# Kernel tuning notes

Measured on AMD Instinct MI355X. Metric: run time of the kernel, lower is better.

The kernel has to match this reference:

```python
import jax, jax.numpy as jnp
import numpy as np

B, T_LAT = 64, 1024
K, PAD = 15, 7
# SMPL-style parents for 24 joints (joint 0 = root)
PARENTS = [0, 0, 0, 0, 1, 2, 3, 4, 5, 6, 7, 8, 9, 9, 9, 12, 13, 14, 16, 17, 18, 19, 20, 21]


def _fine_adjacency():
    # edges of the kinematic tree; +1 virtual root-displacement node (Aberman find_neighbor, dist=1)
    edges = [(PARENTS[j], j) for j in range(1, 24)]  # 23 edges
    n = len(edges) + 1  # 24 graph nodes
    A = np.eye(n, dtype=bool)
    for i, (pi, ci) in enumerate(edges):
        for j, (pj, cj) in enumerate(edges):
            if {pi, ci} & {pj, cj}:
                A[i, j] = True
        if pi == 0 or ci == 0:  # edges touching the root neighbor the virtual root node
            A[i, n - 1] = A[n - 1, i] = True
    return A


def _coarsen(A, pools):
    m = len(pools)
    Ac = np.eye(m, dtype=bool)
    for a in range(m):
        for b in range(m):
            if A[np.ix_(pools[a], pools[b])].any():
                Ac[a, b] = True
    return Ac


def _unpool_weight(pools, n_fine, cpj):
    # SkeletonUnpool: binary matrix copying each coarse joint's channels to its fine members
    W = np.zeros((n_fine * cpj, len(pools) * cpj), np.float32)
    for i, grp in enumerate(pools):
        for j in grp:
            for c in range(cpj):
                W[j * cpj + c, i * cpj + c] = 1.0
    return W


def _conv_mask(A, in_cpj, out_cpj, k):
    n = A.shape[0]
    M = np.zeros((n * out_cpj, n * in_cpj, k), np.float32)
    for a in range(n):
        for b in range(n):
            if A[a, b]:
                M[a * out_cpj:(a + 1) * out_cpj, b * in_cpj:(b + 1) * in_cpj, :] = 1.0
    return M


def _lin_mask(A, in_cpj, out_cpj):
    n = A.shape[0]
    M = np.zeros((n * out_cpj, n * in_cpj), np.float32)
    for a in range(n):
        for b in range(n):
            if A[a, b]:
                M[a * out_cpj:(a + 1) * out_cpj, b * in_cpj:(b + 1) * in_cpj] = 1.0
    return M


def setup_inputs() -> dict:
    key = jax.random.key(0)
    ks = jax.random.split(key, 12)
    A0 = _fine_adjacency()                           # 24 fine graph nodes
    P0 = [[2 * i, 2 * i + 1] for i in range(12)]     # pooling 24 -> 12
    P1 = [[2 * i, 2 * i + 1] for i in range(6)]      # pooling 12 -> 6
    A1 = _coarsen(A0, P0)                            # 12-node coarse adjacency

    inp = {
        'x': jax.random.normal(ks[0], (B, T_LAT, 96), jnp.float32),      # latent: 6 joints x 16 ch
        'offset0': jax.random.normal(ks[1], (B, 12, 3), jnp.float32),
        'offset1': jax.random.normal(ks[2], (B, 24, 3), jnp.float32),
        'W_unpool0': jnp.asarray(_unpool_weight(P1, 12, 16)),            # (192, 96)
        'W_unpool1': jnp.asarray(_unpool_weight(P0, 24, 8)),             # (192, 96)
        'conv_w0': jax.random.normal(ks[3], (96, 192, K), jnp.float32) * 0.05,
        'conv_b0': jax.random.normal(ks[4], (96,), jnp.float32) * 0.05,
        'conv_w1': jax.random.normal(ks[5], (96, 192, K), jnp.float32) * 0.05,
        'conv_b1': jax.random.normal(ks[6], (96,), jnp.float32) * 0.05,
        'off_w0': jax.random.normal(ks[7], (96, 36), jnp.float32) * 0.05,
        'off_b0': jax.random.normal(ks[8], (96,), jnp.float32) * 0.05,
        'off_w1': jax.random.normal(ks[9], (96, 72), jnp.float32) * 0.05,
        'off_b1': jax.random.normal(ks[10], (96,), jnp.float32) * 0.05,
        'conv_mask0': jnp.asarray(_conv_mask(A1, 16, 8, K)),
        'conv_mask1': jnp.asarray(_conv_mask(A0, 8, 4, K)),
        'off_mask0': jnp.asarray(_lin_mask(A1, 3, 8)),
        'off_mask1': jnp.asarray(_lin_mask(A0, 3, 4)),
    }
    return inp


def _upsample2(h):
    # nn.Upsample(scale_factor=2, mode='linear', align_corners=False) on last axis
    b, c, t = h.shape
    return jax.image.resize(h, (b, c, 2 * t), method='linear')


def _conv1d(h, w, b):
    y = jax.lax.conv_general_dilated(h, w, (1,), [(PAD, PAD)],
                                     dimension_numbers=('NCH', 'OIH', 'NCH'))
    return y + b[None, :, None]


def reference(x, offset0, offset1, W_unpool0, W_unpool1,
              conv_w0, conv_b0, conv_w1, conv_b1,
              off_w0, off_b0, off_w1, off_b1,
              conv_mask0, conv_mask1, off_mask0, off_mask1):
    h = jnp.swapaxes(x, -2, -1)                       # (B, C_lat, T)
    # ---- stage 0: upsample time, unpool 6->12 joints, masked conv, offset, LeakyReLU
    h = _upsample2(h)
    h = jnp.einsum('oc,bct->bot', W_unpool0, h)       # (B, 192, 2T)
    h = _conv1d(h, conv_w0 * conv_mask0, conv_b0)     # (B, 96, 2T)
    off = offset0.reshape(offset0.shape[0], -1) @ (off_w0 * off_mask0).T + off_b0
    h = h + off[:, :, None] / 100.0
    h = jax.nn.leaky_relu(h, 0.2)
    # ---- stage 1 (last layer: no activation)
    h = _upsample2(h)
    h = jnp.einsum('oc,bct->bot', W_unpool1, h)       # (B, 192, 4T)
    h = _conv1d(h, conv_w1 * conv_mask1, conv_b1)     # (B, 96, 4T)
    off = offset1.reshape(offset1.shape[0], -1) @ (off_w1 * off_mask1).T + off_b1
    h = h + off[:, :, None] / 100.0
    return h[:, :, :-1]                               # trim last frame
```

## Files before the change

### kernel.cpp

```cpp
#include <hip/hip_runtime.h>

typedef unsigned short ushort_t;
typedef unsigned int u32;
typedef short bf16x8 __attribute__((ext_vector_type(8)));
typedef float f32x4 __attribute__((ext_vector_type(4)));
typedef u32 u32x4 __attribute__((ext_vector_type(4)));

__device__ __forceinline__ float bf2f(ushort_t u) {
    u32 x = ((u32)u) << 16; float f; __builtin_memcpy(&f, &x, 4); return f;
}
__device__ __forceinline__ ushort_t f2bf(float f) {
    u32 x; __builtin_memcpy(&x, &f, 4);
    x = x + 0x7fffu + ((x >> 16) & 1u);
    return (ushort_t)(x >> 16);
}

#define NBB 128
#define UROWS 136
#define USTRB 208
#define UB_BYTES (UROWS * USTRB)
#define LDS_TOTAL UB_BYTES
#define LSTR1 261

__global__ void prepA(const float* __restrict__ w0, const float* __restrict__ m0,
                      const float* __restrict__ w1, const float* __restrict__ m1,
                      const float* __restrict__ offw0, const float* __restrict__ offb0,
                      const float* __restrict__ omask0, const float* __restrict__ convb0,
                      const float* __restrict__ off0,
                      const float* __restrict__ offw1, const float* __restrict__ offb1,
                      const float* __restrict__ omask1, const float* __restrict__ convb1,
                      const float* __restrict__ off1,
                      float* __restrict__ Wplain, float* __restrict__ ADD0,
                      float* __restrict__ ADD1)
{
    int idx = blockIdx.x * 256 + threadIdx.x;
    if (idx < 18432) {
        int o = idx % 96;
        int cc = (idx / 96) % 96;
        int st = idx / 9216;
        const float* w = st ? w1 : w0;
        const float* mk = st ? m1 : m0;
        int cpj = st ? 8 : 16;
        int i = cc / cpj, c = cc % cpj;
        float s[15];
#pragma unroll
        for (int k = 0; k < 15; ++k) s[k] = 0.f;
#pragma unroll
        for (int d = 0; d < 2; ++d) {
            int f = (2 * i + d) * cpj + c;
            int base = (o * 192 + f) * 15;
#pragma unroll
            for (int k = 0; k < 15; ++k)
                s[k] += w[base + k] * mk[base + k];
        }
#pragma unroll
        for (int k = 0; k < 15; ++k)
            Wplain[st * 138240 + (k * 96 + cc) * 96 + o] = s[k];
    } else if (idx < 18432 + 12288) {
        int a = idx - 18432;
        int st = a / 6144; int a2 = a % 6144;
        int o = a2 % 96, b = a2 / 96;
        const float* ow = st ? offw1 : offw0;
        const float* ob = st ? offb1 : offb0;
        const float* om = st ? omask1 : omask0;
        const float* cb = st ? convb1 : convb0;
        const float* of = st ? off1 : off0;
        int J = st ? 72 : 36;
        float s = 0.f;
        for (int j2 = 0; j2 < J; ++j2) s += ow[o * J + j2] * om[o * J + j2] * of[b * J + j2];
        (st ? ADD1 : ADD0)[b * 96 + o] = cb[o] + (s + ob[o]) * 0.01f;
    }
}

__global__ void prepB(const float* __restrict__ Wplain,
                      ushort_t* __restrict__ Wp0, ushort_t* __restrict__ Wp1)
{
    int idx = blockIdx.x * 256 + threadIdx.x;
    if (idx >= 331776) return;
    int o = idx % 96; int t = idx / 96;
    int cc = t % 96; t /= 96;
    int j = t % 9; t /= 9;
    int p = t % 2; int st = t / 2;
    const float* WP = Wplain + (size_t)st * 138240;
    int kk[4]; float cf[4];
    if (p == 0) { kk[0]=2*j;   cf[0]=0.75f; kk[1]=2*j-2; cf[1]=0.25f;
                  kk[2]=2*j+1; cf[2]=0.25f; kk[3]=2*j-1; cf[3]=0.75f; }
    else        { kk[0]=2*j;   cf[0]=0.25f; kk[1]=2*j-2; cf[1]=0.75f;
                  kk[2]=2*j-1; cf[2]=0.75f; kk[3]=2*j-3; cf[3]=0.25f; }
    float s = 0.f;
#pragma unroll
    for (int q = 0; q < 4; ++q) {
        int k = kk[q];
        if (k >= 0 && k < 15) s += cf[q] * WP[(k * 96 + cc) * 96 + o];
    }
    int lane = (o & 15) | (((cc >> 3) & 3) << 4);
    int mh = (o >> 4) / 3, m = (o >> 4) % 3;
    int pos = ((((j * 2 + mh) * 2 + p) * 9) + (cc >> 5) * 3 + m) * 512 + lane * 8 + (cc & 7);
    (st ? Wp1 : Wp0)[pos] = f2bf(s);
}

template<int BF16SRC>
__global__ void prep_G(const float* __restrict__ WP, const float* __restrict__ srcF,
                       const ushort_t* __restrict__ srcB, float* __restrict__ G, int T)
{
    int idx = blockIdx.x * 256 + threadIdx.x;
    if (idx >= 184320) return;
    int o = idx % 96; int t = idx / 96;
    int k = t % 15; t /= 15;
    int side = t % 2; int b = t / 2;
    const float* wk = WP + (size_t)k * 9216 + o;
    int row = side ? T - 1 : 0;
    float s = 0.f;
    if (BF16SRC) {
        const ushort_t* xr = srcB + ((size_t)b * T + row) * 96;
        for (int cc = 0; cc < 96; ++cc)
            s += wk[cc * 96] * bf2f(xr[cc]);
    } else {
        const float* xr = srcF + ((size_t)b * T + row) * 96;
        for (int cc = 0; cc < 96; ++cc)
            s += wk[cc * 96] * bf2f(f2bf(xr[cc]));
    }
    G[((size_t)(b * 96 + o) * 15 + k) * 2 + side] = s;
}

__global__ void prep_cfb(const float* __restrict__ G, float* __restrict__ CF,
                         float* __restrict__ CB)
{
    int idx = blockIdx.x * 256 + threadIdx.x;
    if (idx >= 86016) return;
    int seg = idx % 14; int r = idx / 14;
    int o = r % 96; int b = r / 96;
    bool front = seg < 7; int t = front ? seg : seg - 7;
    float s = 0.f;
    if (front) { for (int k = 0; k <= 6 - t; ++k)   s += G[(((size_t)(b*96+o)*15)+k)*2 + 0]; }
    else       { for (int k = 14 - t; k <= 14; ++k) s += G[(((size_t)(b*96+o)*15)+k)*2 + 1]; }
    (front ? CF : CB)[(b * 7 + t) * 96 + o] = s;
}

template<int STAGE>
__launch_bounds__(256, 4)
__global__ void conv_poly(const float* __restrict__ Xf, const ushort_t* __restrict__ Hbf,
                          const ushort_t* __restrict__ Wp, const float* __restrict__ ADD,
                          const float* __restrict__ CF, const float* __restrict__ CB,
                          ushort_t* __restrict__ Hout, float* __restrict__ Fout, int T)
{
    extern __shared__ char smem[];
    char* Ub = smem;

    const int tid = threadIdx.x;
    const int lane = tid & 63;
    const int wid = tid >> 6;
    const int b = blockIdx.y;
    const int tg = blockIdx.x;
    const int mh = blockIdx.z;
    const int phase = wid & 1;
    const int nq = wid >> 1;
    const int rb0 = tg * NBB - 4;

    const ushort_t* wgl = Wp + (size_t)(mh * 2 + phase) * 4608 + lane * 8;

    if (STAGE == 0) {
        const float* xb = Xf + (size_t)b * T * 96;
        for (int idx = tid; idx < UROWS * 12; idx += 256) {
            int r = idx / 12, q = idx - r * 12;
            int rg = rb0 + r; rg = rg < 0 ? 0 : (rg > T - 1 ? T - 1 : rg);
            const float* src = xb + (size_t)rg * 96 + q * 8;
            float4 a = *(const float4*)src;
            float4 c2 = *(const float4*)(src + 4);
            u32x4 v;
            v[0] = (u32)f2bf(a.x) | ((u32)f2bf(a.y) << 16);
            v[1] = (u32)f2bf(a.z) | ((u32)f2bf(a.w) << 16);
            v[2] = (u32)f2bf(c2.x) | ((u32)f2bf(c2.y) << 16);
            v[3] = (u32)f2bf(c2.z) | ((u32)f2bf(c2.w) << 16);
            *(u32x4*)(Ub + r * USTRB + q * 16) = v;
        }
    } else {
        const ushort_t* xb = Hbf + (size_t)b * T * 96;
        for (int idx = tid; idx < UROWS * 12; idx += 256) {
            int r = idx / 12, q = idx - r * 12;
            int rg = rb0 + r; rg = rg < 0 ? 0 : (rg > T - 1 ? T - 1 : rg);
            u32x4 v = *(const u32x4*)(xb + (size_t)rg * 96 + q * 8);
            *(u32x4*)(Ub + r * USTRB + q * 16) = v;
        }
    }
    __syncthreads();

    f32x4 acc[3][4];
#pragma unroll
    for (int m = 0; m < 3; ++m)
#pragma unroll
        for (int n = 0; n < 4; ++n) acc[m][n] = (f32x4){0.f, 0.f, 0.f, 0.f};

    const int rowbase = 64 * nq + (lane & 15);
    const int og16 = (lane >> 4) * 16;

#pragma unroll
    for (int j = 0; j < 9; ++j) {
        const ushort_t* wj = wgl + (size_t)j * 18432;
        bf16x8 aj[9];
#pragma unroll
        for (int q = 0; q < 9; ++q)
            aj[q] = *(const bf16x8*)(wj + q * 512);

        const int bj = (rowbase + j) * USTRB;
#pragma unroll
        for (int cb = 0; cb < 3; ++cb) {
            const int off0 = bj + cb * 64 + og16;
            bf16x8 bfr[4];
#pragma unroll
            for (int n = 0; n < 4; ++n)
                bfr[n] = *(const bf16x8*)(Ub + off0 + n * 16 * USTRB);
#pragma unroll
            for (int m = 0; m < 3; ++m)
#pragma unroll
                for (int n = 0; n < 4; ++n)
                    acc[m][n] = __builtin_amdgcn_mfma_f32_16x16x32_bf16(aj[cb * 3 + m], bfr[n], acc[m][n], 0, 0, 0);
        }
    }

    const int T2 = 2 * T;
    const int t0 = tg * 2 * NBB;
    const int og4 = (lane >> 4) * 4;

    __syncthreads();

    if (STAGE == 0) {
        ushort_t* L0 = (ushort_t*)Ub;
#pragma unroll
        for (int m = 0; m < 3; ++m) {
            int obase = mh * 48 + m * 16 + og4;
            float addv[4];
#pragma unroll
            for (int rr = 0; rr < 4; ++rr) addv[rr] = ADD[b * 96 + obase + rr];
#pragma unroll
            for (int n = 0; n < 4; ++n) {
                int tl = 2 * (rowbase + 16 * n) + phase;
                int tgl = t0 + tl;
                ushort_t pk[4];
#pragma unroll
                for (int rr = 0; rr < 4; ++rr) {
                    float v = acc[m][n][rr] + addv[rr];
                    if (tgl < 7)                   v -= CF[(b * 7 + tgl) * 96 + obase + rr];
                    if (tgl >= T2 - 7 && tgl < T2) v -= CB[(b * 7 + tgl - (T2 - 7)) * 96 + obase + rr];
                    v = v > 0.f ? v : 0.2f * v;
                    pk[rr] = f2bf(v);
                }
                uint2 w2;
                w2.x = (u32)pk[0] | ((u32)pk[1] << 16);
                w2.y = (u32)pk[2] | ((u32)pk[3] << 16);
                *(uint2*)((char*)L0 + tl * 104 + (m * 16 + og4) * 2) = w2;
            }
        }
        __syncthreads();
        for (int g = tid; g < 256 * 6; g += 256) {
            int row = g / 6, col = g % 6;
            int t = t0 + row;
            if (t < T2) {
                u32x4 v = *(const u32x4*)((char*)L0 + row * 104 + col * 16);
                *(u32x4*)((char*)Hout + ((size_t)(b * T2 + t) * 96 + mh * 48) * 2 + col * 16) = v;
            }
        }
    } else {
        const int TO = T2 - 1;
        float* L1 = (float*)Ub;
#pragma unroll
        for (int m = 0; m < 3; ++m) {
            int obase = mh * 48 + m * 16 + og4;
            float addv[4];
#pragma unroll
            for (int rr = 0; rr < 4; ++rr) addv[rr] = ADD[b * 96 + obase + rr];
#pragma unroll
            for (int n = 0; n < 4; ++n) {
                int tl = 2 * (rowbase + 16 * n) + phase;
                int tgl = t0 + tl;
#pragma unroll
                for (int rr = 0; rr < 4; ++rr) {
                    float v = acc[m][n][rr] + addv[rr];
                    if (tgl < 7)                   v -= CF[(b * 7 + tgl) * 96 + obase + rr];
                    if (tgl >= T2 - 7 && tgl < T2) v -= CB[(b * 7 + tgl - (T2 - 7)) * 96 + obase + rr];
                    L1[(og4 + rr) * LSTR1 + tl] = v;
                }
            }
            __syncthreads();
            for (int g = tid; g < 4096; g += 256) {
                int row = g >> 8, col = g & 255;
                int t = t0 + col;
                if (t < TO) {
                    int o_g = mh * 48 + m * 16 + row;
                    Fout[((size_t)(b * 96 + o_g)) * TO + t] = L1[row * LSTR1 + col];
                }
            }
            __syncthreads();
        }
    }
}

extern "C" void kernel_launch(void* const* d_in, const int* in_sizes, int n_in,
                              void* d_out, int out_size, void* d_ws, size_t ws_size,
                              hipStream_t stream)
{
    const float* x       = (const float*)d_in[0];
    const float* offset0 = (const float*)d_in[1];
    const float* offset1 = (const float*)d_in[2];
    const float* conv_w0 = (const float*)d_in[5];
    const float* conv_b0 = (const float*)d_in[6];
    const float* conv_w1 = (const float*)d_in[7];
    const float* conv_b1 = (const float*)d_in[8];
    const float* off_w0  = (const float*)d_in[9];
    const float* off_b0  = (const float*)d_in[10];
    const float* off_w1  = (const float*)d_in[11];
    const float* off_b1  = (const float*)d_in[12];
    const float* cmask0  = (const float*)d_in[13];
    const float* cmask1  = (const float*)d_in[14];
    const float* omask0  = (const float*)d_in[15];
    const float* omask1  = (const float*)d_in[16];

    char* ws = (char*)d_ws;
    float*    Wplain = (float*)(ws);
    ushort_t* Wp0    = (ushort_t*)(ws + 1105920);
    ushort_t* Wp1    = (ushort_t*)(ws + 1437696);
    float*    ADD0   = (float*)(ws + 1769472);
    float*    ADD1   = (float*)(ws + 1794048);
    float*    CF0    = (float*)(ws + 1818624);
    float*    CB0    = (float*)(ws + 1990656);
    float*    CF1    = (float*)(ws + 2162688);
    float*    CB1    = (float*)(ws + 2334720);
    float*    G0     = (float*)(ws + 2506752);
    float*    G1     = (float*)(ws + 3244032);
    ushort_t* H1     = (ushort_t*)(ws + 3981312);
    float* out = (float*)d_out;

    prepA<<<120, 256, 0, stream>>>(conv_w0, cmask0, conv_w1, cmask1,
                                   off_w0, off_b0, omask0, conv_b0, offset0,
                                   off_w1, off_b1, omask1, conv_b1, offset1,
                                   Wplain, ADD0, ADD1);
    prepB<<<1296, 256, 0, stream>>>(Wplain, Wp0, Wp1);
    prep_G<0><<<720, 256, 0, stream>>>(Wplain, x, nullptr, G0, 1024);
    prep_cfb<<<336, 256, 0, stream>>>(G0, CF0, CB0);

    conv_poly<0><<<dim3(8, 64, 2), 256, LDS_TOTAL, stream>>>(x, nullptr, Wp0, ADD0, CF0, CB0,
                                                             H1, nullptr, 1024);
    prep_G<1><<<720, 256, 0, stream>>>(Wplain + 138240, nullptr, H1, G1, 2048);
    prep_cfb<<<336, 256, 0, stream>>>(G1, CF1, CB1);
    conv_poly<1><<<dim3(16, 64, 2), 256, LDS_TOTAL, stream>>>(nullptr, H1, Wp1, ADD1, CF1, CB1,
                                                              nullptr, out, 2048);
}
```

Measured before the change: 127.3 us.

## Fuse prep kernels, inline boundary corrections, load stage-1 inputs from global directly

```diff
diff --git a/kernel.cpp b/kernel.cpp
--- a/kernel.cpp
+++ b/kernel.cpp
@@ -19,8 +19,8 @@
 #define UROWS 136
 #define USTRB 208
 #define UB_BYTES (UROWS * USTRB)
-#define LDS_TOTAL UB_BYTES
 #define LSTR1 261
+#define LDS1_BYTES (16 * LSTR1 * 4)
 
 __global__ void prepA(const float* __restrict__ w0, const float* __restrict__ m0,
                       const float* __restrict__ w1, const float* __restrict__ m1,
@@ -72,38 +72,12 @@
     }
 }
 
-__global__ void prepB(const float* __restrict__ Wplain,
-                      ushort_t* __restrict__ Wp0, ushort_t* __restrict__ Wp1)
-{
-    int idx = blockIdx.x * 256 + threadIdx.x;
-    if (idx >= 331776) return;
-    int o = idx % 96; int t = idx / 96;
-    int cc = t % 96; t /= 96;
-    int j = t % 9; t /= 9;
-    int p = t % 2; int st = t / 2;
-    const float* WP = Wplain + (size_t)st * 138240;
-    int kk[4]; float cf[4];
-    if (p == 0) { kk[0]=2*j;   cf[0]=0.75f; kk[1]=2*j-2; cf[1]=0.25f;
-                  kk[2]=2*j+1; cf[2]=0.25f; kk[3]=2*j-1; cf[3]=0.75f; }
-    else        { kk[0]=2*j;   cf[0]=0.25f; kk[1]=2*j-2; cf[1]=0.75f;
-                  kk[2]=2*j-1; cf[2]=0.75f; kk[3]=2*j-3; cf[3]=0.25f; }
-    float s = 0.f;
-#pragma unroll
-    for (int q = 0; q < 4; ++q) {
-        int k = kk[q];
-        if (k >= 0 && k < 15) s += cf[q] * WP[(k * 96 + cc) * 96 + o];
-    }
-    int lane = (o & 15) | (((cc >> 3) & 3) << 4);
-    int mh = (o >> 4) / 3, m = (o >> 4) % 3;
-    int pos = ((((j * 2 + mh) * 2 + p) * 9) + (cc >> 5) * 3 + m) * 512 + lane * 8 + (cc & 7);
-    (st ? Wp1 : Wp0)[pos] = f2bf(s);
-}
-
 template<int BF16SRC>
-__global__ void prep_G(const float* __restrict__ WP, const float* __restrict__ srcF,
-                       const ushort_t* __restrict__ srcB, float* __restrict__ G, int T)
-{
-    int idx = blockIdx.x * 256 + threadIdx.x;
+__device__ __forceinline__ void gbody(int idx, const float* __restrict__ WP,
+                                      const float* __restrict__ srcF,
+                                      const ushort_t* __restrict__ srcB,
+                                      float* __restrict__ G, int T)
+{
     if (idx >= 184320) return;
     int o = idx % 96; int t = idx / 96;
     int k = t % 15; t /= 15;
@@ -123,26 +97,63 @@
     G[((size_t)(b * 96 + o) * 15 + k) * 2 + side] = s;
 }
 
-__global__ void prep_cfb(const float* __restrict__ G, float* __restrict__ CF,
-                         float* __restrict__ CB)
-{
+__global__ void prepBG(const float* __restrict__ Wplain,
+                       ushort_t* __restrict__ Wp0, ushort_t* __restrict__ Wp1,
+                       const float* __restrict__ x, float* __restrict__ G0)
+{
+    if (blockIdx.x >= 1296) {
+        gbody<0>((blockIdx.x - 1296) * 256 + threadIdx.x, Wplain, x, nullptr, G0, 1024);
+        return;
+    }
     int idx = blockIdx.x * 256 + threadIdx.x;
-    if (idx >= 86016) return;
-    int seg = idx % 14; int r = idx / 14;
-    int o = r % 96; int b = r / 96;
-    bool front = seg < 7; int t = front ? seg : seg - 7;
+    if (idx >= 331776) return;
+    int o = idx % 96; int t = idx / 96;
+    int cc = t % 96; t /= 96;
+    int j = t % 9; t /= 9;
+    int p = t % 2; int st = t / 2;
+    const float* WP = Wplain + (size_t)st * 138240;
+    int kk[4]; float cf[4];
+    if (p == 0) { kk[0]=2*j;   cf[0]=0.75f; kk[1]=2*j-2; cf[1]=0.25f;
+                  kk[2]=2*j+1; cf[2]=0.25f; kk[3]=2*j-1; cf[3]=0.75f; }
+    else        { kk[0]=2*j;   cf[0]=0.25f; kk[1]=2*j-2; cf[1]=0.75f;
+                  kk[2]=2*j-1; cf[2]=0.75f; kk[3]=2*j-3; cf[3]=0.25f; }
     float s = 0.f;
-    if (front) { for (int k = 0; k <= 6 - t; ++k)   s += G[(((size_t)(b*96+o)*15)+k)*2 + 0]; }
-    else       { for (int k = 14 - t; k <= 14; ++k) s += G[(((size_t)(b*96+o)*15)+k)*2 + 1]; }
-    (front ? CF : CB)[(b * 7 + t) * 96 + o] = s;
-}
-
-template<int STAGE>
+#pragma unroll
+    for (int q = 0; q < 4; ++q) {
+        int k = kk[q];
+        if (k >= 0 && k < 15) s += cf[q] * WP[(k * 96 + cc) * 96 + o];
+    }
+    int lane = (o & 15) | (((cc >> 3) & 3) << 4);
+    int mh = (o >> 4) / 3, m = (o >> 4) % 3;
+    int pos = ((((j * 2 + mh) * 2 + p) * 9) + (cc >> 5) * 3 + m) * 512 + lane * 8 + (cc & 7);
+    (st ? Wp1 : Wp0)[pos] = f2bf(s);
+}
+
+__global__ void prep_G1(const float* __restrict__ WP, const ushort_t* __restrict__ H1,
+                        float* __restrict__ G)
+{
+    gbody<1>(blockIdx.x * 256 + threadIdx.x, WP, nullptr, H1, G, 2048);
+}
+
+__device__ __forceinline__ float bnd_corr(const float* __restrict__ G, int b, int o,
+                                          int tgl, int T2)
+{
+    float s = 0.f;
+    if (tgl < 7) {
+        const float* g = G + ((size_t)(b * 96 + o) * 15) * 2;
+        for (int k = 0; k <= 6 - tgl; ++k) s += g[k * 2];
+    } else if (tgl >= T2 - 7) {
+        int tb = tgl - (T2 - 7);
+        const float* g = G + ((size_t)(b * 96 + o) * 15) * 2 + 1;
+        for (int k = 14 - tb; k <= 14; ++k) s += g[k * 2];
+    }
+    return s;
+}
+
 __launch_bounds__(256, 4)
-__global__ void conv_poly(const float* __restrict__ Xf, const ushort_t* __restrict__ Hbf,
-                          const ushort_t* __restrict__ Wp, const float* __restrict__ ADD,
-                          const float* __restrict__ CF, const float* __restrict__ CB,
-                          ushort_t* __restrict__ Hout, float* __restrict__ Fout, int T)
+__global__ void conv0(const float* __restrict__ Xf, const ushort_t* __restrict__ Wp,
+                      const float* __restrict__ ADD, const float* __restrict__ G,
+                      ushort_t* __restrict__ Hout, int T)
 {
     extern __shared__ char smem[];
     char* Ub = smem;
@@ -159,29 +170,19 @@
 
     const ushort_t* wgl = Wp + (size_t)(mh * 2 + phase) * 4608 + lane * 8;
 
-    if (STAGE == 0) {
-        const float* xb = Xf + (size_t)b * T * 96;
-        for (int idx = tid; idx < UROWS * 12; idx += 256) {
-            int r = idx / 12, q = idx - r * 12;
-            int rg = rb0 + r; rg = rg < 0 ? 0 : (rg > T - 1 ? T - 1 : rg);
-            const float* src = xb + (size_t)rg * 96 + q * 8;
-            float4 a = *(const float4*)src;
-            float4 c2 = *(const float4*)(src + 4);
-            u32x4 v;
-            v[0] = (u32)f2bf(a.x) | ((u32)f2bf(a.y) << 16);
-            v[1] = (u32)f2bf(a.z) | ((u32)f2bf(a.w) << 16);
-            v[2] = (u32)f2bf(c2.x) | ((u32)f2bf(c2.y) << 16);
-            v[3] = (u32)f2bf(c2.z) | ((u32)f2bf(c2.w) << 16);
-            *(u32x4*)(Ub + r * USTRB + q * 16) = v;
-        }
-    } else {
-        const ushort_t* xb = Hbf + (size_t)b * T * 96;
-        for (int idx = tid; idx < UROWS * 12; idx += 256) {
-            int r = idx / 12, q = idx - r * 12;
-            int rg = rb0 + r; rg = rg < 0 ? 0 : (rg > T - 1 ? T - 1 : rg);
-            u32x4 v = *(const u32x4*)(xb + (size_t)rg * 96 + q * 8);
-            *(u32x4*)(Ub + r * USTRB + q * 16) = v;
-        }
+    const float* xb = Xf + (size_t)b * T * 96;
+    for (int idx = tid; idx < UROWS * 12; idx += 256) {
+        int r = idx / 12, q = idx - r * 12;
+        int rg = rb0 + r; rg = rg < 0 ? 0 : (rg > T - 1 ? T - 1 : rg);
+        const float* src = xb + (size_t)rg * 96 + q * 8;
+        float4 a = *(const float4*)src;
+        float4 c2 = *(const float4*)(src + 4);
+        u32x4 v;
+        v[0] = (u32)f2bf(a.x) | ((u32)f2bf(a.y) << 16);
+        v[1] = (u32)f2bf(a.z) | ((u32)f2bf(a.w) << 16);
+        v[2] = (u32)f2bf(c2.x) | ((u32)f2bf(c2.y) << 16);
+        v[3] = (u32)f2bf(c2.z) | ((u32)f2bf(c2.w) << 16);
+        *(u32x4*)(Ub + r * USTRB + q * 16) = v;
     }
     __syncthreads();
 
@@ -224,74 +225,138 @@
 
     __syncthreads();
 
-    if (STAGE == 0) {
-        ushort_t* L0 = (ushort_t*)Ub;
-#pragma unroll
-        for (int m = 0; m < 3; ++m) {
-            int obase = mh * 48 + m * 16 + og4;
-            float addv[4];
-#pragma unroll
-            for (int rr = 0; rr < 4; ++rr) addv[rr] = ADD[b * 96 + obase + rr];
-#pragma unroll
-            for (int n = 0; n < 4; ++n) {
-                int tl = 2 * (rowbase + 16 * n) + phase;
-                int tgl = t0 + tl;
-                ushort_t pk[4];
-#pragma unroll
-                for (int rr = 0; rr < 4; ++rr) {
-                    float v = acc[m][n][rr] + addv[rr];
-                    if (tgl < 7)                   v -= CF[(b * 7 + tgl) * 96 + obase + rr];
-                    if (tgl >= T2 - 7 && tgl < T2) v -= CB[(b * 7 + tgl - (T2 - 7)) * 96 + obase + rr];
-                    v = v > 0.f ? v : 0.2f * v;
-                    pk[rr] = f2bf(v);
-                }
-                uint2 w2;
-                w2.x = (u32)pk[0] | ((u32)pk[1] << 16);
-                w2.y = (u32)pk[2] | ((u32)pk[3] << 16);
-                *(uint2*)((char*)L0 + tl * 104 + (m * 16 + og4) * 2) = w2;
+    ushort_t* L0 = (ushort_t*)Ub;
+#pragma unroll
+    for (int m = 0; m < 3; ++m) {
+        int obase = mh * 48 + m * 16 + og4;
+        float addv[4];
+#pragma unroll
+        for (int rr = 0; rr < 4; ++rr) addv[rr] = ADD[b * 96 + obase + rr];
+#pragma unroll
+        for (int n = 0; n < 4; ++n) {
+            int tl = 2 * (rowbase + 16 * n) + phase;
+            int tgl = t0 + tl;
+            ushort_t pk[4];
+#pragma unroll
+            for (int rr = 0; rr < 4; ++rr) {
+                float v = acc[m][n][rr] + addv[rr];
+                if (tgl < 7 || tgl >= T2 - 7) v -= bnd_corr(G, b, obase + rr, tgl, T2);
+                v = v > 0.f ? v : 0.2f * v;
+                pk[rr] = f2bf(v);
             }
-        }
-        __syncthreads();
-        for (int g = tid; g < 256 * 6; g += 256) {
-            int row = g / 6, col = g % 6;
-            int t = t0 + row;
-            if (t < T2) {
-                u32x4 v = *(const u32x4*)((char*)L0 + row * 104 + col * 16);
-                *(u32x4*)((char*)Hout + ((size_t)(b * T2 + t) * 96 + mh * 48) * 2 + col * 16) = v;
-            }
-        }
-    } else {
-        const int TO = T2 - 1;
-        float* L1 = (float*)Ub;
-#pragma unroll
-        for (int m = 0; m < 3; ++m) {
-            int obase = mh * 48 + m * 16 + og4;
-            float addv[4];
-#pragma unroll
-            for (int rr = 0; rr < 4; ++rr) addv[rr] = ADD[b * 96 + obase + rr];
-#pragma unroll
-            for (int n = 0; n < 4; ++n) {
-                int tl = 2 * (rowbase + 16 * n) + phase;
-                int tgl = t0 + tl;
-#pragma unroll
-                for (int rr = 0; rr < 4; ++rr) {
-                    float v = acc[m][n][rr] + addv[rr];
-                    if (tgl < 7)                   v -= CF[(b * 7 + tgl) * 96 + obase + rr];
-                    if (tgl >= T2 - 7 && tgl < T2) v -= CB[(b * 7 + tgl - (T2 - 7)) * 96 + obase + rr];
-                    L1[(og4 + rr) * LSTR1 + tl] = v;
+            uint2 w2;
+            w2.x = (u32)pk[0] | ((u32)pk[1] << 16);
+            w2.y = (u32)pk[2] | ((u32)pk[3] << 16);
+            *(uint2*)((char*)L0 + tl * 104 + (m * 16 + og4) * 2) = w2;
+        }
+    }
+    __syncthreads();
+    for (int g = tid; g < 256 * 6; g += 256) {
+        int row = g / 6, col = g % 6;
+        int t = t0 + row;
+        if (t < T2) {
+            u32x4 v = *(const u32x4*)((char*)L0 + row * 104 + col * 16);
+            *(u32x4*)((char*)Hout + ((size_t)(b * T2 + t) * 96 + mh * 48) * 2 + col * 16) = v;
+        }
+    }
+}
+
+__launch_bounds__(256, 4)
+__global__ void conv1(const ushort_t* __restrict__ Hbf, const ushort_t* __restrict__ Wp,
+                      const float* __restrict__ ADD, const float* __restrict__ G,
+                      float* __restrict__ Fout, int T)
+{
+    extern __shared__ char smem[];
+
+    const int tid = threadIdx.x;
+    const int lane = tid & 63;
+    const int wid = tid >> 6;
+    const int b = blockIdx.y;
+    const int tg = blockIdx.x;
+    const int mh = blockIdx.z;
+    const int phase = wid & 1;
+    const int nq = wid >> 1;
+    const int rb0 = tg * NBB - 4;
+
+    const ushort_t* wgl = Wp + (size_t)(mh * 2 + phase) * 4608 + lane * 8;
+    const ushort_t* xb = Hbf + (size_t)b * T * 96;
+
+    f32x4 acc[3][4];
+#pragma unroll
+    for (int m = 0; m < 3; ++m)
+#pragma unroll
+        for (int n = 0; n < 4; ++n) acc[m][n] = (f32x4){0.f, 0.f, 0.f, 0.f};
+
+    const int rowbase = 64 * nq + (lane & 15);
+    const int og8 = (lane >> 4) * 8;
+    const int r0 = rb0 + rowbase;
+    const bool safe = (rb0 >= 0) && (rb0 + UROWS <= T);
+
+#pragma unroll
+    for (int j = 0; j < 9; ++j) {
+        const ushort_t* wj = wgl + (size_t)j * 18432;
+        bf16x8 aj[9];
+#pragma unroll
+        for (int q = 0; q < 9; ++q)
+            aj[q] = *(const bf16x8*)(wj + q * 512);
+
+#pragma unroll
+        for (int cb = 0; cb < 3; ++cb) {
+            bf16x8 bfr[4];
+            if (safe) {
+                const ushort_t* rp = xb + (size_t)(r0 + j) * 96 + cb * 32 + og8;
+#pragma unroll
+                for (int n = 0; n < 4; ++n)
+                    bfr[n] = *(const bf16x8*)(rp + n * 16 * 96);
+            } else {
+#pragma unroll
+                for (int n = 0; n < 4; ++n) {
+                    int r = r0 + n * 16 + j;
+                    r = r < 0 ? 0 : (r > T - 1 ? T - 1 : r);
+                    bfr[n] = *(const bf16x8*)(xb + (size_t)r * 96 + cb * 32 + og8);
                 }
             }
-            __syncthreads();
-            for (int g = tid; g < 4096; g += 256) {
-                int row = g >> 8, col = g & 255;
-                int t = t0 + col;
-                if (t < TO) {
-                    int o_g = mh * 48 + m * 16 + row;
-                    Fout[((size_t)(b * 96 + o_g)) * TO + t] = L1[row * LSTR1 + col];
-                }
+#pragma unroll
+            for (int m = 0; m < 3; ++m)
+#pragma unroll
+                for (int n = 0; n < 4; ++n)
+                    acc[m][n] = __builtin_amdgcn_mfma_f32_16x16x32_bf16(aj[cb * 3 + m], bfr[n], acc[m][n], 0, 0, 0);
+        }
+    }
+
+    const int T2 = 2 * T;
+    const int t0 = tg * 2 * NBB;
+    const int og4 = (lane >> 4) * 4;
+    const int TO = T2 - 1;
+
+    float* L1 = (float*)smem;
+#pragma unroll
+    for (int m = 0; m < 3; ++m) {
+        int obase = mh * 48 + m * 16 + og4;
+        float addv[4];
+#pragma unroll
+        for (int rr = 0; rr < 4; ++rr) addv[rr] = ADD[b * 96 + obase + rr];
+#pragma unroll
+        for (int n = 0; n < 4; ++n) {
+            int tl = 2 * (rowbase + 16 * n) + phase;
+            int tgl = t0 + tl;
+#pragma unroll
+            for (int rr = 0; rr < 4; ++rr) {
+                float v = acc[m][n][rr] + addv[rr];
+                if (tgl < 7 || tgl >= T2 - 7) v -= bnd_corr(G, b, obase + rr, tgl, T2);
+                L1[(og4 + rr) * LSTR1 + tl] = v;
             }
-            __syncthreads();
-        }
+        }
+        __syncthreads();
+        for (int g = tid; g < 4096; g += 256) {
+            int row = g >> 8, col = g & 255;
+            int t = t0 + col;
+            if (t < TO) {
+                int o_g = mh * 48 + m * 16 + row;
+                Fout[((size_t)(b * 96 + o_g)) * TO + t] = L1[row * LSTR1 + col];
+            }
+        }
+        __syncthreads();
     }
 }
 
@@ -321,27 +386,18 @@
     ushort_t* Wp1    = (ushort_t*)(ws + 1437696);
     float*    ADD0   = (float*)(ws + 1769472);
     float*    ADD1   = (float*)(ws + 1794048);
-    float*    CF0    = (float*)(ws + 1818624);
-    float*    CB0    = (float*)(ws + 1990656);
-    float*    CF1    = (float*)(ws + 2162688);
-    float*    CB1    = (float*)(ws + 2334720);
-    float*    G0     = (float*)(ws + 2506752);
-    float*    G1     = (float*)(ws + 3244032);
-    ushort_t* H1     = (ushort_t*)(ws + 3981312);
+    float*    G0     = (float*)(ws + 1818624);
+    float*    G1     = (float*)(ws + 2555904);
+    ushort_t* H1     = (ushort_t*)(ws + 3293184);
     float* out = (float*)d_out;
 
     prepA<<<120, 256, 0, stream>>>(conv_w0, cmask0, conv_w1, cmask1,
                                    off_w0, off_b0, omask0, conv_b0, offset0,
                                    off_w1, off_b1, omask1, conv_b1, offset1,
                                    Wplain, ADD0, ADD1);
-    prepB<<<1296, 256, 0, stream>>>(Wplain, Wp0, Wp1);
-    prep_G<0><<<720, 256, 0, stream>>>(Wplain, x, nullptr, G0, 1024);
-    prep_cfb<<<336, 256, 0, stream>>>(G0, CF0, CB0);
-
-    conv_poly<0><<<dim3(8, 64, 2), 256, LDS_TOTAL, stream>>>(x, nullptr, Wp0, ADD0, CF0, CB0,
-                                                             H1, nullptr, 1024);
-    prep_G<1><<<720, 256, 0, stream>>>(Wplain + 138240, nullptr, H1, G1, 2048);
-    prep_cfb<<<336, 256, 0, stream>>>(G1, CF1, CB1);
-    conv_poly<1><<<dim3(16, 64, 2), 256, LDS_TOTAL, stream>>>(nullptr, H1, Wp1, ADD1, CF1, CB1,
-                                                              nullptr, out, 2048);
-}
+    prepBG<<<2016, 256, 0, stream>>>(Wplain, Wp0, Wp1, x, G0);
+
+    conv0<<<dim3(8, 64, 2), 256, UB_BYTES, stream>>>(x, Wp0, ADD0, G0, H1, 1024);
+    prep_G1<<<720, 256, 0, stream>>>(Wplain + 138240, H1, G1);
+    conv1<<<dim3(16, 64, 2), 256, LDS1_BYTES, stream>>>(H1, Wp1, ADD1, G1, out, 2048);
+}
```

Measured after the change: 189.3 us. +48.7%, slower.
